# Optimization experiments

Hardware: AMD Instinct MI355X
Metric: run time of the kernel (lower is better)

## Reference

```python
import jax, jax.numpy as jnp
import numpy as np

N_NODES = 100000
N_EDGES = 1600000
D = 128
R = 3
L = 3


def setup_inputs() -> dict:
    key = jax.random.key(0)
    ks = jax.random.split(key, 6)
    features = jax.random.normal(ks[0], (N_NODES, D), dtype=jnp.float32)
    # per-layer relation weights [L, R, D, D], self-loop weights [L, D, D], bias [L, D]
    W = jax.random.normal(ks[1], (L, R, D, D), dtype=jnp.float32) * 0.05
    W_self = jax.random.normal(ks[2], (L, D, D), dtype=jnp.float32) * 0.05
    bias = jnp.zeros((L, D), dtype=jnp.float32)
    src = jax.random.randint(ks[3], (N_EDGES,), 0, N_NODES, dtype=jnp.int32)
    dst = jax.random.randint(ks[4], (N_EDGES,), 0, N_NODES, dtype=jnp.int32)
    etypes = jax.random.randint(ks[5], (N_EDGES,), 0, R, dtype=jnp.int32)
    return {"features": features, "W": W, "W_self": W_self, "bias": bias,
            "src": src, "dst": dst, "etypes": etypes}


def _rel_graph_conv(h, Wl, Wsl, bl, src, dst, etypes):
    # Transform all nodes under every relation once: [N, R, D]
    xW = jnp.einsum('ni,rio->nro', h, Wl)
    # Per-edge message = transformed source feature under edge's relation: [E, D]
    msg = xW[src, etypes]
    # Scatter-add aggregation onto destination nodes
    agg = jax.ops.segment_sum(msg, dst, num_segments=N_NODES)
    # Self-loop + bias (DGL RelGraphConv defaults: self_loop=True, bias=True)
    return agg + h @ Wsl + bl


def reference(features, W, W_self, bias, src, dst, etypes):
    h = features
    for l in range(L):
        h = _rel_graph_conv(h, W[l], W_self[l], bias[l], src, dst, etypes)
    return h
```

## Files before the change

### kernel.cpp

```cpp
#include <hip/hip_runtime.h>


#define DD 128

typedef __attribute__((ext_vector_type(8))) short short8;
typedef __attribute__((ext_vector_type(4))) float f32x4;

__device__ __forceinline__ float bf2f(ushort u) {
    return __uint_as_float(((unsigned)u) << 16);
}
__device__ __forceinline__ ushort f2bf(float f) {
    unsigned b = __float_as_uint(f);
    return (ushort)((b + 0x7FFFu + ((b >> 16) & 1u)) >> 16);
}
__device__ __forceinline__ void splitbf(float f, ushort& hi, ushort& lo) {
    hi = f2bf(f);
    lo = f2bf(f - bf2f(hi));
}

#define GLOAD_LDS16(g, l)                                                      \
    __builtin_amdgcn_global_load_lds(                                          \
        (const __attribute__((address_space(1))) void*)(g),                    \
        (__attribute__((address_space(3))) void*)(l), 16, 0, 0)

__global__ __launch_bounds__(256) void k_split_feat(
    const float* __restrict__ feat, ushort* __restrict__ h_hi,
    ushort* __restrict__ h_lo, int n4)
{
    int i = blockIdx.x * 256 + threadIdx.x;
    if (i >= n4) return;
    float4 v = reinterpret_cast<const float4*>(feat)[i];
    ushort4 hh, ll;
    splitbf(v.x, hh.x, ll.x); splitbf(v.y, hh.y, ll.y);
    splitbf(v.z, hh.z, ll.z); splitbf(v.w, hh.w, ll.w);
    reinterpret_cast<ushort4*>(h_hi)[i] = hh;
    reinterpret_cast<ushort4*>(h_lo)[i] = ll;
}

__global__ __launch_bounds__(256) void k_build_bimg(
    const float* __restrict__ W, const float* __restrict__ Wself,
    ushort* __restrict__ bh, ushort* __restrict__ bl_)
{
    int idx = blockIdx.x * 256 + threadIdx.x;
    if (idx >= 3 * 65536) return;
    int l = idx >> 16, rem = idx & 65535;
    int j = rem & 7, v = (rem >> 3) & 63, g = (rem >> 9) & 7, c = (rem >> 12) & 15;
    int col = g * 16 + (v & 15);
    int k = c * 32 + ((v >> 4) * 8) + j;
    float val;
    if (k < 128) val = Wself[((size_t)l * 128 + k) * 128 + col];
    else {
        int kk = k - 128, r = kk >> 7, i = kk & 127;
        val = W[(((size_t)l * 3 + r) * 128 + i) * 128 + col];
    }
    ushort hi, lo; splitbf(val, hi, lo);
    bh[idx] = hi; bl_[idx] = lo;
}

__global__ __launch_bounds__(256) void k_zero(int* __restrict__ p, int n) {
    int i = blockIdx.x * 256 + threadIdx.x;
    if (i < n) p[i] = 0;
}
__global__ __launch_bounds__(256) void k_hist3(
    const int* __restrict__ dst, const int* __restrict__ et,
    int* __restrict__ deg, int nEdges) {
    int e = blockIdx.x * 256 + threadIdx.x;
    if (e < nEdges) atomicAdd(&deg[dst[e] * 3 + et[e]], 1);
}
__global__ __launch_bounds__(1024) void k_scanA(
    const int* __restrict__ deg, int* __restrict__ off,
    int* __restrict__ chunkSum, int n) {
    __shared__ int s[1024];
    const int tid = threadIdx.x;
    const int i = blockIdx.x * 1024 + tid;
    int v = (i < n) ? deg[i] : 0;
    s[tid] = v;
    __syncthreads();
    for (int o = 1; o < 1024; o <<= 1) {
        int t = (tid >= o) ? s[tid - o] : 0;
        __syncthreads();
        s[tid] += t;
        __syncthreads();
    }
    if (i < n) off[i] = s[tid] - v;
    if (tid == 1023) chunkSum[blockIdx.x] = s[1023];
}
__global__ __launch_bounds__(512) void k_scanB(int* __restrict__ chunkSum, int nChunks) {
    __shared__ int s[512];
    const int tid = threadIdx.x;
    int v = (tid < nChunks) ? chunkSum[tid] : 0;
    s[tid] = v;
    __syncthreads();
    for (int o = 1; o < 512; o <<= 1) {
        int t = (tid >= o) ? s[tid - o] : 0;
        __syncthreads();
        s[tid] += t;
        __syncthreads();
    }
    if (tid < nChunks) chunkSum[tid] = s[tid] - v;
}
__global__ __launch_bounds__(256) void k_scanC(
    int* __restrict__ off, int* __restrict__ pos,
    const int* __restrict__ chunkBase, int n, int total) {
    int i = blockIdx.x * 256 + threadIdx.x;
    if (i < n) {
        int o = off[i] + chunkBase[i >> 10];
        off[i] = o;
        pos[i] = o;
    }
    if (i == 0) off[n] = total;
}
__global__ __launch_bounds__(256) void k_scatter3(
    const int* __restrict__ src, const int* __restrict__ dst,
    const int* __restrict__ et, int* __restrict__ pos,
    int* __restrict__ csr, int nEdges) {
    int e = blockIdx.x * 256 + threadIdx.x;
    if (e < nEdges) {
        int j = atomicAdd(&pos[dst[e] * 3 + et[e]], 1);
        csr[j] = src[e];
    }
}

__global__ __launch_bounds__(256) void rgcn_gather(
    const ushort* __restrict__ h_hi, const ushort* __restrict__ h_lo,
    const int* __restrict__ off3, const int* __restrict__ csr,
    ushort* __restrict__ aggF_hi, ushort* __restrict__ aggF_lo,
    int nNodes)
{
    const int gtid = blockIdx.x * 256 + threadIdx.x;
    const int gw   = gtid >> 6;
    const int lane = threadIdx.x & 63;
    const int sub  = lane >> 5;
    const int li   = lane & 31;
    const int n    = gw * 2 + sub;
    if (n >= nNodes) return;
    const int e0 = li * 4;

    #pragma unroll
    for (int r = 0; r < 3; ++r) {
        const int b = off3[n * 3 + r];
        const int e = off3[n * 3 + r + 1];
        float ax = 0.f, ay = 0.f, az = 0.f, aw = 0.f;
        int j = b;
        for (; j + 3 < e; j += 4) {
            int s0 = csr[j], s1 = csr[j + 1], s2 = csr[j + 2], s3 = csr[j + 3];
            ushort4 h0 = *reinterpret_cast<const ushort4*>(h_hi + (size_t)s0 * DD + e0);
            ushort4 l0 = *reinterpret_cast<const ushort4*>(h_lo + (size_t)s0 * DD + e0);
            ushort4 h1 = *reinterpret_cast<const ushort4*>(h_hi + (size_t)s1 * DD + e0);
            ushort4 l1 = *reinterpret_cast<const ushort4*>(h_lo + (size_t)s1 * DD + e0);
            ushort4 h2 = *reinterpret_cast<const ushort4*>(h_hi + (size_t)s2 * DD + e0);
            ushort4 l2 = *reinterpret_cast<const ushort4*>(h_lo + (size_t)s2 * DD + e0);
            ushort4 h3 = *reinterpret_cast<const ushort4*>(h_hi + (size_t)s3 * DD + e0);
            ushort4 l3 = *reinterpret_cast<const ushort4*>(h_lo + (size_t)s3 * DD + e0);
            ax += (bf2f(h0.x) + bf2f(l0.x)) + (bf2f(h1.x) + bf2f(l1.x))
                + (bf2f(h2.x) + bf2f(l2.x)) + (bf2f(h3.x) + bf2f(l3.x));
            ay += (bf2f(h0.y) + bf2f(l0.y)) + (bf2f(h1.y) + bf2f(l1.y))
                + (bf2f(h2.y) + bf2f(l2.y)) + (bf2f(h3.y) + bf2f(l3.y));
            az += (bf2f(h0.z) + bf2f(l0.z)) + (bf2f(h1.z) + bf2f(l1.z))
                + (bf2f(h2.z) + bf2f(l2.z)) + (bf2f(h3.z) + bf2f(l3.z));
            aw += (bf2f(h0.w) + bf2f(l0.w)) + (bf2f(h1.w) + bf2f(l1.w))
                + (bf2f(h2.w) + bf2f(l2.w)) + (bf2f(h3.w) + bf2f(l3.w));
        }
        for (; j < e; ++j) {
            int s0 = csr[j];
            ushort4 h0 = *reinterpret_cast<const ushort4*>(h_hi + (size_t)s0 * DD + e0);
            ushort4 l0 = *reinterpret_cast<const ushort4*>(h_lo + (size_t)s0 * DD + e0);
            ax += bf2f(h0.x) + bf2f(l0.x);
            ay += bf2f(h0.y) + bf2f(l0.y);
            az += bf2f(h0.z) + bf2f(l0.z);
            aw += bf2f(h0.w) + bf2f(l0.w);
        }
        const size_t o = ((size_t)n * 3 + r) * DD + e0;
        ushort4 hh, ll;
        splitbf(ax, hh.x, ll.x); splitbf(ay, hh.y, ll.y);
        splitbf(az, hh.z, ll.z); splitbf(aw, hh.w, ll.w);
        *reinterpret_cast<ushort4*>(aggF_hi + o) = hh;
        *reinterpret_cast<ushort4*>(aggF_lo + o) = ll;
    }
}

__global__ __launch_bounds__(256) void rgcn_mfma(
    const ushort* __restrict__ h_hi, const ushort* __restrict__ h_lo,
    const ushort* __restrict__ aggF_hi, const ushort* __restrict__ aggF_lo,
    const ushort* __restrict__ bimg_hi, const ushort* __restrict__ bimg_lo,
    const float* __restrict__ bl,
    ushort* __restrict__ out_hi, ushort* __restrict__ out_lo,
    float* __restrict__ out_f32,
    int isFinal, int nNodes)
{
    __shared__ ushort Ah[2][4096];
    __shared__ ushort Al[2][4096];

    const int t = threadIdx.x;
    const int w = t >> 6;
    const int lane = t & 63;
    const int wr = w >> 1, wc = w & 1;
    const int row0 = blockIdx.x * 128;

    f32x4 acc[4][4];
    #pragma unroll
    for (int i = 0; i < 4; ++i)
        #pragma unroll
        for (int jn = 0; jn < 4; ++jn) acc[i][jn] = f32x4{0.f, 0.f, 0.f, 0.f};

    const int arow0 = row0 + (2 * w) * 16 + (lane & 15);
    const int arow1 = row0 + (2 * w + 1) * 16 + (lane & 15);
    const int asub  = (lane >> 4) * 8;

#define STAGE_A(CH, BUF)                                                          \
    {                                                                             \
        const int kc_ = (CH) * 32;                                                \
        const ushort* sH_; const ushort* sL_; size_t stride_; int kloc_;          \
        if (kc_ < 128) { sH_ = h_hi; sL_ = h_lo; stride_ = DD;  kloc_ = kc_; }    \
        else { sH_ = aggF_hi; sL_ = aggF_lo; stride_ = 384; kloc_ = kc_ - 128; }  \
        GLOAD_LDS16(sH_ + (size_t)arow0 * stride_ + kloc_ + asub, &Ah[BUF][(2 * w) * 512]);     \
        GLOAD_LDS16(sH_ + (size_t)arow1 * stride_ + kloc_ + asub, &Ah[BUF][(2 * w + 1) * 512]); \
        GLOAD_LDS16(sL_ + (size_t)arow0 * stride_ + kloc_ + asub, &Al[BUF][(2 * w) * 512]);     \
        GLOAD_LDS16(sL_ + (size_t)arow1 * stride_ + kloc_ + asub, &Al[BUF][(2 * w + 1) * 512]); \
    }

    STAGE_A(0, 0);
    __syncthreads();

    for (int ch = 0; ch < 16; ++ch) {
        const int cur = ch & 1;
        if (ch < 15) STAGE_A(ch + 1, cur ^ 1);

        short8 bh[4], blo[4];
        #pragma unroll
        for (int jn = 0; jn < 4; ++jn) {
            const size_t base = ((size_t)(ch * 8 + wc * 4 + jn) * 64 + lane) * 8;
            bh[jn]  = *reinterpret_cast<const short8*>(bimg_hi + base);
            blo[jn] = *reinterpret_cast<const short8*>(bimg_lo + base);
        }
        short8 ah[4], al[4];
        #pragma unroll
        for (int i = 0; i < 4; ++i) {
            const int mt = wr * 4 + i;
            ah[i] = *reinterpret_cast<const short8*>(&Ah[cur][mt * 512 + lane * 8]);
            al[i] = *reinterpret_cast<const short8*>(&Al[cur][mt * 512 + lane * 8]);
        }
        #pragma unroll
        for (int i = 0; i < 4; ++i)
            #pragma unroll
            for (int jn = 0; jn < 4; ++jn) {
                acc[i][jn] = __builtin_amdgcn_mfma_f32_16x16x32_bf16(ah[i], bh[jn],  acc[i][jn], 0, 0, 0);
                acc[i][jn] = __builtin_amdgcn_mfma_f32_16x16x32_bf16(ah[i], blo[jn], acc[i][jn], 0, 0, 0);
                acc[i][jn] = __builtin_amdgcn_mfma_f32_16x16x32_bf16(al[i], bh[jn],  acc[i][jn], 0, 0, 0);
            }
        __syncthreads();
    }
#undef STAGE_A

    const int colb = wc * 64 + (lane & 15);
    const int rowb = row0 + wr * 64 + (lane >> 4) * 4;
    #pragma unroll
    for (int i = 0; i < 4; ++i) {
        #pragma unroll
        for (int jn = 0; jn < 4; ++jn) {
            const int col = colb + jn * 16;
            const float bb = bl[col];
            #pragma unroll
            for (int rr = 0; rr < 4; ++rr) {
                const int row = rowb + i * 16 + rr;
                if (row < nNodes) {
                    const float v = acc[i][jn][rr] + bb;
                    if (isFinal) {
                        out_f32[(size_t)row * DD + col] = v;
                    } else {
                        ushort hi, lo; splitbf(v, hi, lo);
                        out_hi[(size_t)row * DD + col] = hi;
                        out_lo[(size_t)row * DD + col] = lo;
                    }
                }
            }
        }
    }
}

extern "C" void kernel_launch(void* const* d_in, const int* in_sizes, int n_in,
                              void* d_out, int out_size, void* d_ws, size_t ws_size,
                              hipStream_t stream) {
    const float* feat  = (const float*)d_in[0];
    const float* W     = (const float*)d_in[1];
    const float* Wself = (const float*)d_in[2];
    const float* bias  = (const float*)d_in[3];
    const int*   src   = (const int*)d_in[4];
    const int*   dst   = (const int*)d_in[5];
    const int*   et    = (const int*)d_in[6];
    float* out = (float*)d_out;

    const int nNodes = in_sizes[0] / DD;
    const int nEdges = in_sizes[4];
    const int nBins  = nNodes * 3;

    ushort* h_hi    = (ushort*)d_ws;
    ushort* h_lo    = h_hi + (size_t)nNodes * DD;
    ushort* aggF_hi = h_lo + (size_t)nNodes * DD;
    ushort* aggF_lo = aggF_hi + (size_t)nNodes * 384;
    ushort* bimg_hi = aggF_lo + (size_t)nNodes * 384;
    ushort* bimg_lo = bimg_hi + 3 * 65536;
    int* ip = (int*)(bimg_lo + 3 * 65536);
    int* deg3     = ip;
    int* off3     = deg3 + nBins;
    int* pos3     = off3 + nBins + 1;
    int* chunkSum = pos3 + nBins;
    int* csr      = chunkSum + 512;

    const int nChunks = (nBins + 1023) / 1024;
    const int nEB = (nEdges + 255) / 256;
    const int nBB = (nBins + 255) / 256;

    const int n4 = nNodes * DD / 4;
    k_split_feat<<<(n4 + 255) / 256, 256, 0, stream>>>(feat, h_hi, h_lo, n4);
    k_build_bimg<<<(3 * 65536 + 255) / 256, 256, 0, stream>>>(W, Wself, bimg_hi, bimg_lo);

    k_zero    <<<nBB, 256, 0, stream>>>(deg3, nBins);
    k_hist3   <<<nEB, 256, 0, stream>>>(dst, et, deg3, nEdges);
    k_scanA   <<<nChunks, 1024, 0, stream>>>(deg3, off3, chunkSum, nBins);
    k_scanB   <<<1, 512, 0, stream>>>(chunkSum, nChunks);
    k_scanC   <<<nBB, 256, 0, stream>>>(off3, pos3, chunkSum, nBins, nEdges);
    k_scatter3<<<nEB, 256, 0, stream>>>(src, dst, et, pos3, csr, nEdges);

    const int gatherBlocks = (nNodes + 7) / 8;
    const int gemmBlocks   = (nNodes + 127) / 128;

    for (int l = 0; l < 3; ++l) {
        rgcn_gather<<<gatherBlocks, 256, 0, stream>>>(
            h_hi, h_lo, off3, csr, aggF_hi, aggF_lo, nNodes);
        rgcn_mfma<<<gemmBlocks, 256, 0, stream>>>(
            h_hi, h_lo, aggF_hi, aggF_lo,
            bimg_hi + l * 65536, bimg_lo + l * 65536,
            bias + (size_t)l * DD,
            h_hi, h_lo, out, (l == 2) ? 1 : 0, nNodes);
    }
}
```

Baseline: 918.2 us.

## Interleave bf16 hi/lo split planes into packed 32-bit words

Stores node features and aggregated messages as interleaved hi/lo bf16 pairs in one 32-bit word instead of two separate planes. The gather kernel then issues one 16-byte load per source row instead of two 8-byte loads, and the GEMM stages a single LDS buffer, unpacking hi/lo with bit operations before the MFMAs. Aggregate and final output stores become nontemporal. The unpack adds ALU work in the GEMM inner loop, and the mixed-precision split and total bytes moved stay the same.

```diff
diff --git a/kernel.cpp b/kernel.cpp
--- a/kernel.cpp
+++ b/kernel.cpp
@@ -5,6 +5,7 @@
 
 typedef __attribute__((ext_vector_type(8))) short short8;
 typedef __attribute__((ext_vector_type(4))) float f32x4;
+typedef __attribute__((ext_vector_type(4))) unsigned int u32x4;
 
 __device__ __forceinline__ float bf2f(ushort u) {
     return __uint_as_float(((unsigned)u) << 16);
@@ -13,10 +14,14 @@
     unsigned b = __float_as_uint(f);
     return (ushort)((b + 0x7FFFu + ((b >> 16) & 1u)) >> 16);
 }
-__device__ __forceinline__ void splitbf(float f, ushort& hi, ushort& lo) {
-    hi = f2bf(f);
-    lo = f2bf(f - bf2f(hi));
-}
+__device__ __forceinline__ unsigned packbf(float f) {
+    ushort hi = f2bf(f);
+    ushort lo = f2bf(f - bf2f(hi));
+    return (unsigned)hi | ((unsigned)lo << 16);
+}
+__device__ __forceinline__ float hi_f(unsigned u) { return __uint_as_float(u << 16); }
+__device__ __forceinline__ float lo_f(unsigned u) { return __uint_as_float(u & 0xffff0000u); }
+__device__ __forceinline__ float both_f(unsigned u) { return hi_f(u) + lo_f(u); }
 
 #define GLOAD_LDS16(g, l)                                                      \
     __builtin_amdgcn_global_load_lds(                                          \
@@ -24,17 +29,14 @@
         (__attribute__((address_space(3))) void*)(l), 16, 0, 0)
 
 __global__ __launch_bounds__(256) void k_split_feat(
-    const float* __restrict__ feat, ushort* __restrict__ h_hi,
-    ushort* __restrict__ h_lo, int n4)
+    const float* __restrict__ feat, unsigned* __restrict__ h_il, int n4)
 {
     int i = blockIdx.x * 256 + threadIdx.x;
     if (i >= n4) return;
     float4 v = reinterpret_cast<const float4*>(feat)[i];
-    ushort4 hh, ll;
-    splitbf(v.x, hh.x, ll.x); splitbf(v.y, hh.y, ll.y);
-    splitbf(v.z, hh.z, ll.z); splitbf(v.w, hh.w, ll.w);
-    reinterpret_cast<ushort4*>(h_hi)[i] = hh;
-    reinterpret_cast<ushort4*>(h_lo)[i] = ll;
+    u32x4 p;
+    p.x = packbf(v.x); p.y = packbf(v.y); p.z = packbf(v.z); p.w = packbf(v.w);
+    reinterpret_cast<u32x4*>(h_il)[i] = p;
 }
 
 __global__ __launch_bounds__(256) void k_build_bimg(
@@ -53,7 +55,8 @@
         int kk = k - 128, r = kk >> 7, i = kk & 127;
         val = W[(((size_t)l * 3 + r) * 128 + i) * 128 + col];
     }
-    ushort hi, lo; splitbf(val, hi, lo);
+    ushort hi = f2bf(val);
+    ushort lo = f2bf(val - bf2f(hi));
     bh[idx] = hi; bl_[idx] = lo;
 }
 
@@ -122,9 +125,9 @@
 }
 
 __global__ __launch_bounds__(256) void rgcn_gather(
-    const ushort* __restrict__ h_hi, const ushort* __restrict__ h_lo,
+    const unsigned* __restrict__ h_il,
     const int* __restrict__ off3, const int* __restrict__ csr,
-    ushort* __restrict__ aggF_hi, ushort* __restrict__ aggF_lo,
+    unsigned* __restrict__ aggF_il,
     int nNodes)
 {
     const int gtid = blockIdx.x * 256 + threadIdx.x;
@@ -144,52 +147,38 @@
         int j = b;
         for (; j + 3 < e; j += 4) {
             int s0 = csr[j], s1 = csr[j + 1], s2 = csr[j + 2], s3 = csr[j + 3];
-            ushort4 h0 = *reinterpret_cast<const ushort4*>(h_hi + (size_t)s0 * DD + e0);
-            ushort4 l0 = *reinterpret_cast<const ushort4*>(h_lo + (size_t)s0 * DD + e0);
-            ushort4 h1 = *reinterpret_cast<const ushort4*>(h_hi + (size_t)s1 * DD + e0);
-            ushort4 l1 = *reinterpret_cast<const ushort4*>(h_lo + (size_t)s1 * DD + e0);
-            ushort4 h2 = *reinterpret_cast<const ushort4*>(h_hi + (size_t)s2 * DD + e0);
-            ushort4 l2 = *reinterpret_cast<const ushort4*>(h_lo + (size_t)s2 * DD + e0);
-            ushort4 h3 = *reinterpret_cast<const ushort4*>(h_hi + (size_t)s3 * DD + e0);
-            ushort4 l3 = *reinterpret_cast<const ushort4*>(h_lo + (size_t)s3 * DD + e0);
-            ax += (bf2f(h0.x) + bf2f(l0.x)) + (bf2f(h1.x) + bf2f(l1.x))
-                + (bf2f(h2.x) + bf2f(l2.x)) + (bf2f(h3.x) + bf2f(l3.x));
-            ay += (bf2f(h0.y) + bf2f(l0.y)) + (bf2f(h1.y) + bf2f(l1.y))
-                + (bf2f(h2.y) + bf2f(l2.y)) + (bf2f(h3.y) + bf2f(l3.y));
-            az += (bf2f(h0.z) + bf2f(l0.z)) + (bf2f(h1.z) + bf2f(l1.z))
-                + (bf2f(h2.z) + bf2f(l2.z)) + (bf2f(h3.z) + bf2f(l3.z));
-            aw += (bf2f(h0.w) + bf2f(l0.w)) + (bf2f(h1.w) + bf2f(l1.w))
-                + (bf2f(h2.w) + bf2f(l2.w)) + (bf2f(h3.w) + bf2f(l3.w));
+            u32x4 v0 = *reinterpret_cast<const u32x4*>(h_il + (size_t)s0 * DD + e0);
+            u32x4 v1 = *reinterpret_cast<const u32x4*>(h_il + (size_t)s1 * DD + e0);
+            u32x4 v2 = *reinterpret_cast<const u32x4*>(h_il + (size_t)s2 * DD + e0);
+            u32x4 v3 = *reinterpret_cast<const u32x4*>(h_il + (size_t)s3 * DD + e0);
+            ax += (both_f(v0.x) + both_f(v1.x)) + (both_f(v2.x) + both_f(v3.x));
+            ay += (both_f(v0.y) + both_f(v1.y)) + (both_f(v2.y) + both_f(v3.y));
+            az += (both_f(v0.z) + both_f(v1.z)) + (both_f(v2.z) + both_f(v3.z));
+            aw += (both_f(v0.w) + both_f(v1.w)) + (both_f(v2.w) + both_f(v3.w));
         }
         for (; j < e; ++j) {
             int s0 = csr[j];
-            ushort4 h0 = *reinterpret_cast<const ushort4*>(h_hi + (size_t)s0 * DD + e0);
-            ushort4 l0 = *reinterpret_cast<const ushort4*>(h_lo + (size_t)s0 * DD + e0);
-            ax += bf2f(h0.x) + bf2f(l0.x);
-            ay += bf2f(h0.y) + bf2f(l0.y);
-            az += bf2f(h0.z) + bf2f(l0.z);
-            aw += bf2f(h0.w) + bf2f(l0.w);
-        }
-        const size_t o = ((size_t)n * 3 + r) * DD + e0;
-        ushort4 hh, ll;
-        splitbf(ax, hh.x, ll.x); splitbf(ay, hh.y, ll.y);
-        splitbf(az, hh.z, ll.z); splitbf(aw, hh.w, ll.w);
-        *reinterpret_cast<ushort4*>(aggF_hi + o) = hh;
-        *reinterpret_cast<ushort4*>(aggF_lo + o) = ll;
+            u32x4 v0 = *reinterpret_cast<const u32x4*>(h_il + (size_t)s0 * DD + e0);
+            ax += both_f(v0.x); ay += both_f(v0.y);
+            az += both_f(v0.z); aw += both_f(v0.w);
+        }
+        u32x4 p;
+        p.x = packbf(ax); p.y = packbf(ay); p.z = packbf(az); p.w = packbf(aw);
+        __builtin_nontemporal_store(
+            p, reinterpret_cast<u32x4*>(aggF_il + (size_t)n * 384 + r * DD + e0));
     }
 }
 
 __global__ __launch_bounds__(256) void rgcn_mfma(
-    const ushort* __restrict__ h_hi, const ushort* __restrict__ h_lo,
-    const ushort* __restrict__ aggF_hi, const ushort* __restrict__ aggF_lo,
+    const unsigned* __restrict__ h_il,
+    const unsigned* __restrict__ aggF_il,
     const ushort* __restrict__ bimg_hi, const ushort* __restrict__ bimg_lo,
     const float* __restrict__ bl,
-    ushort* __restrict__ out_hi, ushort* __restrict__ out_lo,
+    unsigned* __restrict__ out_il,
     float* __restrict__ out_f32,
     int isFinal, int nNodes)
 {
-    __shared__ ushort Ah[2][4096];
-    __shared__ ushort Al[2][4096];
+    __shared__ unsigned As[2][4096];
 
     const int t = threadIdx.x;
     const int w = t >> 6;
@@ -205,18 +194,20 @@
 
     const int arow0 = row0 + (2 * w) * 16 + (lane & 15);
     const int arow1 = row0 + (2 * w + 1) * 16 + (lane & 15);
-    const int asub  = (lane >> 4) * 8;
-
-#define STAGE_A(CH, BUF)                                                          \
-    {                                                                             \
-        const int kc_ = (CH) * 32;                                                \
-        const ushort* sH_; const ushort* sL_; size_t stride_; int kloc_;          \
-        if (kc_ < 128) { sH_ = h_hi; sL_ = h_lo; stride_ = DD;  kloc_ = kc_; }    \
-        else { sH_ = aggF_hi; sL_ = aggF_lo; stride_ = 384; kloc_ = kc_ - 128; }  \
-        GLOAD_LDS16(sH_ + (size_t)arow0 * stride_ + kloc_ + asub, &Ah[BUF][(2 * w) * 512]);     \
-        GLOAD_LDS16(sH_ + (size_t)arow1 * stride_ + kloc_ + asub, &Ah[BUF][(2 * w + 1) * 512]); \
-        GLOAD_LDS16(sL_ + (size_t)arow0 * stride_ + kloc_ + asub, &Al[BUF][(2 * w) * 512]);     \
-        GLOAD_LDS16(sL_ + (size_t)arow1 * stride_ + kloc_ + asub, &Al[BUF][(2 * w + 1) * 512]); \
+    const int ak    = (lane >> 4) * 8;
+
+#define STAGE_A(CH, BUF)                                                           \
+    {                                                                              \
+        const int kc_ = (CH) * 32;                                                 \
+        const unsigned* sP_; int strideU_; int kloc_;                              \
+        if (kc_ < 128) { sP_ = h_il; strideU_ = DD; kloc_ = kc_; }                 \
+        else { sP_ = aggF_il; strideU_ = 384; kloc_ = kc_ - 128; }                 \
+        const unsigned* s0_ = sP_ + (size_t)arow0 * strideU_ + kloc_ + ak;         \
+        const unsigned* s1_ = sP_ + (size_t)arow1 * strideU_ + kloc_ + ak;         \
+        GLOAD_LDS16(s0_,     &As[BUF][(2 * w) * 512]);                             \
+        GLOAD_LDS16(s0_ + 4, &As[BUF][(2 * w) * 512 + 256]);                       \
+        GLOAD_LDS16(s1_,     &As[BUF][(2 * w + 1) * 512]);                         \
+        GLOAD_LDS16(s1_ + 4, &As[BUF][(2 * w + 1) * 512 + 256]);                   \
     }
 
     STAGE_A(0, 0);
@@ -236,9 +227,20 @@
         short8 ah[4], al[4];
         #pragma unroll
         for (int i = 0; i < 4; ++i) {
-            const int mt = wr * 4 + i;
-            ah[i] = *reinterpret_cast<const short8*>(&Ah[cur][mt * 512 + lane * 8]);
-            al[i] = *reinterpret_cast<const short8*>(&Al[cur][mt * 512 + lane * 8]);
+            const unsigned* tb = &As[cur][(wr * 4 + i) * 512];
+            u32x4 q0 = *reinterpret_cast<const u32x4*>(tb + lane * 4);
+            u32x4 q1 = *reinterpret_cast<const u32x4*>(tb + 256 + lane * 4);
+            u32x4 AH, AL;
+            AH.x = (q0.x & 0xffffu) | (q0.y << 16);
+            AH.y = (q0.z & 0xffffu) | (q0.w << 16);
+            AH.z = (q1.x & 0xffffu) | (q1.y << 16);
+            AH.w = (q1.z & 0xffffu) | (q1.w << 16);
+            AL.x = (q0.x >> 16) | (q0.y & 0xffff0000u);
+            AL.y = (q0.z >> 16) | (q0.w & 0xffff0000u);
+            AL.z = (q1.x >> 16) | (q1.y & 0xffff0000u);
+            AL.w = (q1.z >> 16) | (q1.w & 0xffff0000u);
+            ah[i] = __builtin_bit_cast(short8, AH);
+            al[i] = __builtin_bit_cast(short8, AL);
         }
         #pragma unroll
         for (int i = 0; i < 4; ++i)
@@ -266,11 +268,9 @@
                 if (row < nNodes) {
                     const float v = acc[i][jn][rr] + bb;
                     if (isFinal) {
-                        out_f32[(size_t)row * DD + col] = v;
+                        __builtin_nontemporal_store(v, out_f32 + (size_t)row * DD + col);
                     } else {
-                        ushort hi, lo; splitbf(v, hi, lo);
-                        out_hi[(size_t)row * DD + col] = hi;
-                        out_lo[(size_t)row * DD + col] = lo;
+                        out_il[(size_t)row * DD + col] = packbf(v);
                     }
                 }
             }
@@ -294,12 +294,10 @@
     const int nEdges = in_sizes[4];
     const int nBins  = nNodes * 3;
 
-    ushort* h_hi    = (ushort*)d_ws;
-    ushort* h_lo    = h_hi + (size_t)nNodes * DD;
-    ushort* aggF_hi = h_lo + (size_t)nNodes * DD;
-    ushort* aggF_lo = aggF_hi + (size_t)nNodes * 384;
-    ushort* bimg_hi = aggF_lo + (size_t)nNodes * 384;
-    ushort* bimg_lo = bimg_hi + 3 * 65536;
+    unsigned* h_il    = (unsigned*)d_ws;
+    unsigned* aggF_il = h_il + (size_t)nNodes * DD;
+    ushort* bimg_hi   = (ushort*)(aggF_il + (size_t)nNodes * 384);
+    ushort* bimg_lo   = bimg_hi + 3 * 65536;
     int* ip = (int*)(bimg_lo + 3 * 65536);
     int* deg3     = ip;
     int* off3     = deg3 + nBins;
@@ -312,7 +310,7 @@
     const int nBB = (nBins + 255) / 256;
 
     const int n4 = nNodes * DD / 4;
-    k_split_feat<<<(n4 + 255) / 256, 256, 0, stream>>>(feat, h_hi, h_lo, n4);
+    k_split_feat<<<(n4 + 255) / 256, 256, 0, stream>>>(feat, h_il, n4);
     k_build_bimg<<<(3 * 65536 + 255) / 256, 256, 0, stream>>>(W, Wself, bimg_hi, bimg_lo);
 
     k_zero    <<<nBB, 256, 0, stream>>>(deg3, nBins);
@@ -327,11 +325,11 @@
 
     for (int l = 0; l < 3; ++l) {
         rgcn_gather<<<gatherBlocks, 256, 0, stream>>>(
-            h_hi, h_lo, off3, csr, aggF_hi, aggF_lo, nNodes);
+            h_il, off3, csr, aggF_il, nNodes);
         rgcn_mfma<<<gemmBlocks, 256, 0, stream>>>(
-            h_hi, h_lo, aggF_hi, aggF_lo,
+            h_il, aggF_il,
             bimg_hi + l * 65536, bimg_lo + l * 65536,
             bias + (size_t)l * DD,
-            h_hi, h_lo, out, (l == 2) ? 1 : 0, nNodes);
-    }
-}
+            h_il, out, (l == 2) ? 1 : 0, nNodes);
+    }
+}
```

Measured after the change: 904.0 us. About the same (-1.5%).
